# Kernel optimization log

Measured on AMD Instinct MI355X. Metric: run time of the kernel, lower is better.

## Reference

```python
import jax, jax.numpy as jnp
import numpy as np


def setup_inputs() -> dict:
    key = jax.random.key(0)
    ks = jax.random.split(key, 4)
    B, Tq, Tv, D = 8, 256, 512, 256  # decoder_dim = D = 256
    query = jax.random.normal(ks[0], (B, Tq, D), dtype=jnp.float32)
    value = jax.random.normal(ks[1], (B, Tv, D), dtype=jnp.float32)
    W1 = jax.random.normal(ks[2], (D, D), dtype=jnp.float32) * (1.0 / np.sqrt(D))
    b1 = jnp.zeros((D,), dtype=jnp.float32)
    W2 = jax.random.normal(ks[3], (D, D), dtype=jnp.float32) * (1.0 / np.sqrt(D))
    b2 = jnp.zeros((D,), dtype=jnp.float32)
    return {"query": query, "value": value, "W1": W1, "b1": b1, "W2": W2, "b2": b2}


def reference(query, value, W1, b1, W2, b2):
    # Dense projections: [B,Tq,D], [B,Tv,D]
    q = jnp.einsum('bqd,de->bqe', query, W1) + b1
    v = jnp.einsum('bvd,de->bve', value, W2) + b2
    # Additive (Bahdanau) score: broadcast tanh then reduce over feature dim
    # score: [B,Tq,Tv]  (intermediate [B,Tq,Tv,D] is the fusion target)
    score = jnp.tanh(q[:, :, None, :] + v[:, None, :, :]).sum(axis=-1)
    alignment = jax.nn.softmax(score, axis=-1)  # [B,Tq,Tv]
    context = jnp.einsum('bqv,bvd->bqd', alignment, value)  # [B,Tq,D]
    context = jnp.concatenate([context, query], axis=-1)  # [B,Tq,2D]
    alignment_t = jnp.transpose(alignment, (0, 2, 1))  # [B,Tv,Tq]
    return context, alignment_t
```

## Files before the change

### kernel.cpp

```cpp
#include <hip/hip_runtime.h>

#define B_  8
#define TQ  256
#define TV  512
#define DD  256

__device__ __forceinline__ float fast_exp2(float x) {
#if __has_builtin(__builtin_amdgcn_exp2f)
  return __builtin_amdgcn_exp2f(x);
#else
  return __exp2f(x);
#endif
}
__device__ __forceinline__ float fast_rcp(float x) {
#if __has_builtin(__builtin_amdgcn_rcpf)
  return __builtin_amdgcn_rcpf(x);
#else
  return 1.0f / x;
#endif
}

__global__ __launch_bounds__(256) void proj_fused(
    const float* __restrict__ query, const float* __restrict__ value,
    const float* __restrict__ W1, const float* __restrict__ b1,
    const float* __restrict__ W2, const float* __restrict__ b2,
    float* __restrict__ qp, float* __restrict__ vp, float scale) {
  __shared__ float As[2][32][64];
  __shared__ float Bs[2][32][64];
  const int t  = threadIdx.x;
  const int rt = blockIdx.x;
  const int bn = blockIdx.y << 6;

  const float* A; const float* W; const float* bias; float* out; int row0;
  if (rt < 32) { row0 = rt << 6;        A = query; W = W1; bias = b1; out = qp; }
  else         { row0 = (rt - 32) << 6; A = value; W = W2; bias = b2; out = vp; }

  const int tx = t & 15, ty = t >> 4;
  const int aar = t >> 3, aac = (t & 7) << 2;
  const int bbr = t >> 4, bbc = (t & 15) << 2;

  float4 ra[2], rb[2];
#pragma unroll
  for (int it = 0; it < 2; ++it) {
    ra[it] = *(const float4*)(A + (size_t)(row0 + (it << 5) + aar) * DD + aac);
    rb[it] = *(const float4*)(W + (size_t)((it << 4) + bbr) * DD + bn + bbc);
  }
#pragma unroll
  for (int it = 0; it < 2; ++it) {
    const int m = (it << 5) + aar;
#pragma unroll
    for (int c = 0; c < 4; ++c) {
      const int k = aac + c;
      As[0][k][m ^ (((k >> 2) & 7) << 2)] = (&ra[it].x)[c];
    }
    *(float4*)&Bs[0][(it << 4) + bbr][bbc] = rb[it];
  }
  __syncthreads();

  float acc[4][4] = {{0.f,0.f,0.f,0.f},{0.f,0.f,0.f,0.f},
                     {0.f,0.f,0.f,0.f},{0.f,0.f,0.f,0.f}};
  int p = 0;

  for (int k0 = 0; k0 < 256; k0 += 32) {
    const bool more = (k0 + 32) < 256;
    if (more) {
#pragma unroll
      for (int it = 0; it < 2; ++it) {
        ra[it] = *(const float4*)(A + (size_t)(row0 + (it << 5) + aar) * DD + k0 + 32 + aac);
        rb[it] = *(const float4*)(W + (size_t)(k0 + 32 + (it << 4) + bbr) * DD + bn + bbc);
      }
    }
#pragma unroll
    for (int k = 0; k < 32; ++k) {
      float4 aq = *(const float4*)&As[p][k][(ty << 2) ^ (((k >> 2) & 7) << 2)];
      float4 bq = *(const float4*)&Bs[p][k][tx << 2];
      acc[0][0] = fmaf(aq.x, bq.x, acc[0][0]); acc[0][1] = fmaf(aq.x, bq.y, acc[0][1]);
      acc[0][2] = fmaf(aq.x, bq.z, acc[0][2]); acc[0][3] = fmaf(aq.x, bq.w, acc[0][3]);
      acc[1][0] = fmaf(aq.y, bq.x, acc[1][0]); acc[1][1] = fmaf(aq.y, bq.y, acc[1][1]);
      acc[1][2] = fmaf(aq.y, bq.z, acc[1][2]); acc[1][3] = fmaf(aq.y, bq.w, acc[1][3]);
      acc[2][0] = fmaf(aq.z, bq.x, acc[2][0]); acc[2][1] = fmaf(aq.z, bq.y, acc[2][1]);
      acc[2][2] = fmaf(aq.z, bq.z, acc[2][2]); acc[2][3] = fmaf(aq.z, bq.w, acc[2][3]);
      acc[3][0] = fmaf(aq.w, bq.x, acc[3][0]); acc[3][1] = fmaf(aq.w, bq.y, acc[3][1]);
      acc[3][2] = fmaf(aq.w, bq.z, acc[3][2]); acc[3][3] = fmaf(aq.w, bq.w, acc[3][3]);
    }
    if (more) {
      const int q = p ^ 1;
#pragma unroll
      for (int it = 0; it < 2; ++it) {
        const int m = (it << 5) + aar;
#pragma unroll
        for (int c = 0; c < 4; ++c) {
          const int k = aac + c;
          As[q][k][m ^ (((k >> 2) & 7) << 2)] = (&ra[it].x)[c];
        }
        *(float4*)&Bs[q][(it << 4) + bbr][bbc] = rb[it];
      }
      __syncthreads();
      p = q;
    }
  }

  float4 bvv = *(const float4*)&bias[bn + (tx << 2)];
#pragma unroll
  for (int r = 0; r < 4; ++r) {
    float4 o;
    o.x = fast_exp2(scale * (acc[r][0] + bvv.x));
    o.y = fast_exp2(scale * (acc[r][1] + bvv.y));
    o.z = fast_exp2(scale * (acc[r][2] + bvv.z));
    o.w = fast_exp2(scale * (acc[r][3] + bvv.w));
    *(float4*)(out + (size_t)(row0 + (ty << 2) + r) * DD + bn + (tx << 2)) = o;
  }
}

__global__ __launch_bounds__(512, 4) void attn_kernel(
    const float* __restrict__ qp, const float* __restrict__ vp,
    const float* __restrict__ value, const float* __restrict__ query,
    float* __restrict__ out1, float* __restrict__ out2) {
  __shared__ float vs2[2][512 * 20];
  float* alg = &vs2[0][0];

  const int t    = threadIdx.x;
  const int lane = t & 63;
  const int wv   = t >> 6;
  const int bb   = blockIdx.x & 7;
  const int i0   = (blockIdx.x >> 3) << 2;
  const int jrow = (wv << 6) + lane;

  const float* vpb = vp + (size_t)bb * TV * DD;
  const float* qb  = qp + (size_t)(bb * TQ + i0) * DD;

  const int sj = t >> 2;
  const int sc = (t & 3) << 2;

  float acc[4] = {0.f, 0.f, 0.f, 0.f};

#pragma unroll
  for (int k = 0; k < 4; ++k) {
    const int j = (k << 7) + sj;
    float4 x = *(const float4*)(vpb + (size_t)j * DD + sc);
    *(float4*)&vs2[0][j * 20 + sc] = x;
  }
  __syncthreads();

#pragma unroll 1
  for (int s = 0; s < 16; ++s) {
    float4 r0, r1, r2, r3;
    if (s < 15) {
      const int dn = (s + 1) << 4;
      r0 = *(const float4*)(vpb + (size_t)(sj)       * DD + dn + sc);
      r1 = *(const float4*)(vpb + (size_t)(128 + sj) * DD + dn + sc);
      r2 = *(const float4*)(vpb + (size_t)(256 + sj) * DD + dn + sc);
      r3 = *(const float4*)(vpb + (size_t)(384 + sj) * DD + dn + sc);
    }

    const float* vrow = &vs2[s & 1][jrow * 20];
    const int dbase = s << 4;
#pragma unroll
    for (int d4 = 0; d4 < 4; ++d4) {
      float4 v4 = *(const float4*)&vrow[d4 << 2];
#pragma unroll
      for (int i = 0; i < 4; ++i) {
        float4 q4 = *(const float4*)(qb + i * DD + dbase + (d4 << 2));
        float a = q4.x * v4.x, b = q4.y * v4.y;
        float c = q4.z * v4.z, d = q4.w * v4.w;
        float sab = a + b,  scd = c + d;
        float Q1 = fmaf(a, b, sab + 1.f);
        float Q2 = fmaf(c, d, scd + 1.f);
        float P1 = sab + 2.f, P2 = scd + 2.f;
        float N  = fmaf(P2, Q1, P1 * Q2);
        acc[i] = fmaf(N, fast_rcp(Q1 * Q2), acc[i]);
      }
    }

    if (s < 15) {
      const int nb = (s + 1) & 1;
      *(float4*)&vs2[nb][(sj)       * 20 + sc] = r0;
      *(float4*)&vs2[nb][(128 + sj) * 20 + sc] = r1;
      *(float4*)&vs2[nb][(256 + sj) * 20 + sc] = r2;
      *(float4*)&vs2[nb][(384 + sj) * 20 + sc] = r3;
    }
    __syncthreads();
  }

#pragma unroll
  for (int i = 0; i < 4; ++i) alg[(i << 9) + jrow] = acc[i];
  __syncthreads();

  if (wv < 4) {
    float s[8];
#pragma unroll
    for (int c = 0; c < 8; ++c) s[c] = alg[(wv << 9) + (c << 6) + lane];
    float mn = s[0];
#pragma unroll
    for (int c = 1; c < 8; ++c) mn = fminf(mn, s[c]);
#pragma unroll
    for (int m = 1; m < 64; m <<= 1) mn = fminf(mn, __shfl_xor(mn, m, 64));

    const float CC = 2.8853900817779268f;
    float p[8];
    float sum = 0.f;
#pragma unroll
    for (int c = 0; c < 8; ++c) { p[c] = fast_exp2(CC * (mn - s[c])); sum += p[c]; }
#pragma unroll
    for (int m = 1; m < 64; m <<= 1) sum += __shfl_xor(sum, m, 64);
    const float inv = fast_rcp(sum);
#pragma unroll
    for (int c = 0; c < 8; ++c) alg[(wv << 9) + (c << 6) + lane] = p[c] * inv;
  }
  __syncthreads();

  {
    const int j = t;
    float4 av = make_float4(alg[j], alg[512 + j], alg[1024 + j], alg[1536 + j]);
    *(float4*)(out2 + (size_t)(bb * TV + j) * TQ + i0) = av;
  }

  const int f  = t & 255;
  const int rp = t >> 8;
  float c0 = 0.f, c1 = 0.f;
  const float* vb = value + (size_t)bb * TV * DD;
  const float* a0p = &alg[((rp << 1) + 0) << 9];
  const float* a1p = &alg[((rp << 1) + 1) << 9];
#pragma unroll 4
  for (int j = 0; j < TV; j += 4) {
    float v0 = vb[(size_t)(j + 0) * DD + f];
    float v1 = vb[(size_t)(j + 1) * DD + f];
    float v2 = vb[(size_t)(j + 2) * DD + f];
    float v3 = vb[(size_t)(j + 3) * DD + f];
    float4 a0 = *(const float4*)&a0p[j];
    float4 a1 = *(const float4*)&a1p[j];
    c0 += a0.x * v0 + a0.y * v1 + a0.z * v2 + a0.w * v3;
    c1 += a1.x * v0 + a1.y * v1 + a1.z * v2 + a1.w * v3;
  }

  const int r0_ = (rp << 1), r1_ = r0_ + 1;
  const float* qg = query + (size_t)(bb * TQ + i0) * DD;
  float* o = out1 + (size_t)(bb * TQ + i0) * (2 * DD);
  o[r0_ * 512 + f] = c0; o[r0_ * 512 + 256 + f] = qg[r0_ * DD + f];
  o[r1_ * 512 + f] = c1; o[r1_ * 512 + 256 + f] = qg[r1_ * DD + f];
}

extern "C" void kernel_launch(void* const* d_in, const int* in_sizes, int n_in,
                              void* d_out, int out_size, void* d_ws, size_t ws_size,
                              hipStream_t stream) {
  const float* query = (const float*)d_in[0];
  const float* value = (const float*)d_in[1];
  const float* W1    = (const float*)d_in[2];
  const float* b1    = (const float*)d_in[3];
  const float* W2    = (const float*)d_in[4];
  const float* b2    = (const float*)d_in[5];

  float* out1 = (float*)d_out;
  float* out2 = out1 + (size_t)B_ * TQ * 2 * DD;

  float* qp = (float*)d_ws;
  float* vp = qp + (size_t)B_ * TQ * DD;

  const float SC = 2.8853900817779268f;

  proj_fused<<<dim3(96, 4), 256, 0, stream>>>(query, value, W1, b1, W2, b2, qp, vp, SC);
  attn_kernel<<<dim3(B_ * (TQ / 4)), 512, 0, stream>>>(qp, vp, value, query, out1, out2);
}
```

Measured before the change: 139.1 us.

## Halve queries per attention block, single-buffer LDS, split context over keys

Each attention block now handles 2 query rows instead of 4, which doubles the grid. The value-projection tile in LDS is single-buffered with an extra barrier per step, cutting shared memory so more blocks can be resident per CU. The context matmul splits the key dimension across the two thread halves and reduces the partial sums through LDS. In exchange, each loaded projected-value element is reused by fewer queries, so global/L2 reads of vp roughly double, and the loss of double buffering adds synchronization stalls.

```diff
diff --git a/kernel.cpp b/kernel.cpp
--- a/kernel.cpp
+++ b/kernel.cpp
@@ -112,19 +112,19 @@
   }
 }
 
-__global__ __launch_bounds__(512, 4) void attn_kernel(
+__global__ __launch_bounds__(512, 8) void attn_kernel(
     const float* __restrict__ qp, const float* __restrict__ vp,
     const float* __restrict__ value, const float* __restrict__ query,
     float* __restrict__ out1, float* __restrict__ out2) {
-  __shared__ float vs2[2][512 * 20];
-  float* alg = &vs2[0][0];
+  __shared__ float vs[512 * 20];
+  float* alg = vs;
+  float* part = vs + 2048;
 
   const int t    = threadIdx.x;
   const int lane = t & 63;
   const int wv   = t >> 6;
   const int bb   = blockIdx.x & 7;
-  const int i0   = (blockIdx.x >> 3) << 2;
-  const int jrow = (wv << 6) + lane;
+  const int i0   = (blockIdx.x >> 3) << 1;
 
   const float* vpb = vp + (size_t)bb * TV * DD;
   const float* qb  = qp + (size_t)(bb * TQ + i0) * DD;
@@ -132,13 +132,13 @@
   const int sj = t >> 2;
   const int sc = (t & 3) << 2;
 
-  float acc[4] = {0.f, 0.f, 0.f, 0.f};
+  float acc0 = 0.f, acc1 = 0.f;
 
 #pragma unroll
   for (int k = 0; k < 4; ++k) {
     const int j = (k << 7) + sj;
     float4 x = *(const float4*)(vpb + (size_t)j * DD + sc);
-    *(float4*)&vs2[0][j * 20 + sc] = x;
+    *(float4*)&vs[j * 20 + sc] = x;
   }
   __syncthreads();
 
@@ -153,13 +153,13 @@
       r3 = *(const float4*)(vpb + (size_t)(384 + sj) * DD + dn + sc);
     }
 
-    const float* vrow = &vs2[s & 1][jrow * 20];
+    const float* vrow = &vs[t * 20];
     const int dbase = s << 4;
 #pragma unroll
     for (int d4 = 0; d4 < 4; ++d4) {
       float4 v4 = *(const float4*)&vrow[d4 << 2];
 #pragma unroll
-      for (int i = 0; i < 4; ++i) {
+      for (int i = 0; i < 2; ++i) {
         float4 q4 = *(const float4*)(qb + i * DD + dbase + (d4 << 2));
         float a = q4.x * v4.x, b = q4.y * v4.y;
         float c = q4.z * v4.z, d = q4.w * v4.w;
@@ -168,25 +168,25 @@
         float Q2 = fmaf(c, d, scd + 1.f);
         float P1 = sab + 2.f, P2 = scd + 2.f;
         float N  = fmaf(P2, Q1, P1 * Q2);
-        acc[i] = fmaf(N, fast_rcp(Q1 * Q2), acc[i]);
+        float r  = fmaf(N, fast_rcp(Q1 * Q2), (i == 0) ? acc0 : acc1);
+        if (i == 0) acc0 = r; else acc1 = r;
       }
     }
-
+    __syncthreads();
     if (s < 15) {
-      const int nb = (s + 1) & 1;
-      *(float4*)&vs2[nb][(sj)       * 20 + sc] = r0;
-      *(float4*)&vs2[nb][(128 + sj) * 20 + sc] = r1;
-      *(float4*)&vs2[nb][(256 + sj) * 20 + sc] = r2;
-      *(float4*)&vs2[nb][(384 + sj) * 20 + sc] = r3;
-    }
-    __syncthreads();
-  }
-
-#pragma unroll
-  for (int i = 0; i < 4; ++i) alg[(i << 9) + jrow] = acc[i];
-  __syncthreads();
-
-  if (wv < 4) {
+      *(float4*)&vs[(sj)       * 20 + sc] = r0;
+      *(float4*)&vs[(128 + sj) * 20 + sc] = r1;
+      *(float4*)&vs[(256 + sj) * 20 + sc] = r2;
+      *(float4*)&vs[(384 + sj) * 20 + sc] = r3;
+      __syncthreads();
+    }
+  }
+
+  alg[t]       = acc0;
+  alg[512 + t] = acc1;
+  __syncthreads();
+
+  if (wv < 2) {
     float s[8];
 #pragma unroll
     for (int c = 0; c < 8; ++c) s[c] = alg[(wv << 9) + (c << 6) + lane];
@@ -211,33 +211,38 @@
 
   {
     const int j = t;
-    float4 av = make_float4(alg[j], alg[512 + j], alg[1024 + j], alg[1536 + j]);
-    *(float4*)(out2 + (size_t)(bb * TV + j) * TQ + i0) = av;
+    float2 av = make_float2(alg[j], alg[512 + j]);
+    *(float2*)(out2 + (size_t)(bb * TV + j) * TQ + i0) = av;
   }
 
   const int f  = t & 255;
-  const int rp = t >> 8;
+  const int jh = t >> 8;
   float c0 = 0.f, c1 = 0.f;
   const float* vb = value + (size_t)bb * TV * DD;
-  const float* a0p = &alg[((rp << 1) + 0) << 9];
-  const float* a1p = &alg[((rp << 1) + 1) << 9];
+  const int jbeg = jh << 8;
 #pragma unroll 4
-  for (int j = 0; j < TV; j += 4) {
+  for (int j = jbeg; j < jbeg + 256; j += 4) {
     float v0 = vb[(size_t)(j + 0) * DD + f];
     float v1 = vb[(size_t)(j + 1) * DD + f];
     float v2 = vb[(size_t)(j + 2) * DD + f];
     float v3 = vb[(size_t)(j + 3) * DD + f];
-    float4 a0 = *(const float4*)&a0p[j];
-    float4 a1 = *(const float4*)&a1p[j];
+    float4 a0 = *(const float4*)&alg[j];
+    float4 a1 = *(const float4*)&alg[512 + j];
     c0 += a0.x * v0 + a0.y * v1 + a0.z * v2 + a0.w * v3;
     c1 += a1.x * v0 + a1.y * v1 + a1.z * v2 + a1.w * v3;
   }
-
-  const int r0_ = (rp << 1), r1_ = r0_ + 1;
-  const float* qg = query + (size_t)(bb * TQ + i0) * DD;
-  float* o = out1 + (size_t)(bb * TQ + i0) * (2 * DD);
-  o[r0_ * 512 + f] = c0; o[r0_ * 512 + 256 + f] = qg[r0_ * DD + f];
-  o[r1_ * 512 + f] = c1; o[r1_ * 512 + 256 + f] = qg[r1_ * DD + f];
+  part[(jh << 9) + f]       = c0;
+  part[(jh << 9) + 256 + f] = c1;
+  __syncthreads();
+
+  {
+    const int row = jh;
+    const float cfull = part[(row << 8) + f] + part[512 + (row << 8) + f];
+    const float* qg = query + (size_t)(bb * TQ + i0) * DD;
+    float* o = out1 + (size_t)(bb * TQ + i0) * (2 * DD);
+    o[row * 512 + f]       = cfull;
+    o[row * 512 + 256 + f] = qg[row * DD + f];
+  }
 }
 
 extern "C" void kernel_launch(void* const* d_in, const int* in_sizes, int n_in,
@@ -259,5 +264,5 @@
   const float SC = 2.8853900817779268f;
 
   proj_fused<<<dim3(96, 4), 256, 0, stream>>>(query, value, W1, b1, W2, b2, qp, vp, SC);
-  attn_kernel<<<dim3(B_ * (TQ / 4)), 512, 0, stream>>>(qp, vp, value, query, out1, out2);
-}
+  attn_kernel<<<dim3(B_ * (TQ / 2)), 512, 0, stream>>>(qp, vp, value, query, out1, out2);
+}
```

Result: slower. 219.3 us (+57.7%).
